# Kernel optimization log

Hardware: AMD Instinct MI355X
Metric: run time of the kernel (lower is better)

Reference implementation:

```python
import jax, jax.numpy as jnp
import numpy as np

B, T, V, H = 32, 512, 1024, 256

def setup_inputs() -> dict:
    key = jax.random.key(0)
    k = jax.random.split(key, 6)
    glorot_x = (6.0 / (V + H)) ** 0.5
    glorot_h = (6.0 / (H + H)) ** 0.5
    glorot_d = (6.0 / (H + V)) ** 0.5
    return {
        "X": jax.random.normal(k[0], (B, T, V), dtype=jnp.float32),
        "Wx": jax.random.uniform(k[1], (V, H), jnp.float32, -glorot_x, glorot_x),
        "Wh": jax.random.uniform(k[2], (H, H), jnp.float32, -glorot_h, glorot_h),
        "b": jnp.zeros((H,), jnp.float32),
        "Wd": jax.random.uniform(k[3], (H, V), jnp.float32, -glorot_d, glorot_d),
        "bd": jnp.zeros((V,), jnp.float32),
    }

def reference(X, Wx, Wh, b, Wd, bd):
    # Precompute input projections for all timesteps: [T, B, H]
    xproj = jnp.einsum('btv,vh->tbh', X, Wx) + b
    h0 = jnp.zeros((X.shape[0], Wh.shape[0]), X.dtype)

    def step(h, xp):
        h_new = jnp.tanh(xp + h @ Wh)  # SimpleRNNCell: tanh(Wx x + Wh h + b)
        return h_new, h_new

    new_state, Ys = jax.lax.scan(step, h0, xproj)  # Ys: [T, B, H]
    Y = jnp.transpose(Ys, (1, 0, 2)).reshape(-1, Wh.shape[0])  # [B*T, H]
    out = jax.nn.softmax(Y @ Wd + bd, axis=-1)  # [B*T, V]
    return out, new_state
```

## Files before the change

### kernel.cpp

```cpp
#include <hip/hip_runtime.h>

typedef float f32x4 __attribute__((ext_vector_type(4)));
typedef float f32x2 __attribute__((ext_vector_type(2)));
typedef _Float16 f16x8 __attribute__((ext_vector_type(8)));
typedef _Float16 f16x4 __attribute__((ext_vector_type(4)));
typedef _Float16 f16x2 __attribute__((ext_vector_type(2)));

__device__ __forceinline__ float tanh_fast(float x) {
  float e = __builtin_amdgcn_exp2f(x * 2.885390081777927f);
  return 1.0f - 2.0f * __builtin_amdgcn_rcpf(e + 1.0f);
}

__global__ __launch_bounds__(256) void k_transpose_cast(
    const float* __restrict__ in, _Float16* __restrict__ outp, int R, int C)
{
  __shared__ float tile[32][33];
  const int tx = threadIdx.x & 31, ty = threadIdx.x >> 5;
  const int tc = blockIdx.x * 32, tr = blockIdx.y * 32;
#pragma unroll
  for (int i = 0; i < 32; i += 8)
    tile[ty + i][tx] = in[(size_t)(tr + ty + i) * C + tc + tx];
  __syncthreads();
#pragma unroll
  for (int i = 0; i < 32; i += 8)
    outp[(size_t)(tc + ty + i) * R + tr + tx] = (_Float16)tile[tx][ty + i];
}

__global__ __launch_bounds__(256) void k_transpose_cast_perm(
    const float* __restrict__ in, _Float16* __restrict__ outp, int R, int C)
{
  __shared__ float tile[32][33];
  const int tx = threadIdx.x & 31, ty = threadIdx.x >> 5;
  const int tc = blockIdx.x * 32, tr = blockIdx.y * 32;
#pragma unroll
  for (int i = 0; i < 32; i += 8)
    tile[ty + i][tx] = in[(size_t)(tr + ty + i) * C + tc + tx];
  __syncthreads();
  const int r = tr + tx;
  const int p = (r & ~31) | ((r & 15) << 1) | ((r >> 4) & 1);
#pragma unroll
  for (int i = 0; i < 32; i += 8)
    outp[(size_t)(tc + ty + i) * R + p] = (_Float16)tile[tx][ty + i];
}

__global__ __launch_bounds__(256) void k_gemm1(
    const float* __restrict__ X, const _Float16* __restrict__ WxT,
    const float* __restrict__ bias, float* __restrict__ xp_packed)
{
  __shared__ _Float16 As[32][72];
  __shared__ _Float16 Bs[256][72];
  const int tid = threadIdx.x;
  const int lane = tid & 63, w = tid >> 6;
  const int l15 = lane & 15, lq = lane >> 4;
  const int m0 = blockIdx.x * 32;
  const int wm = w & 1, wn = w >> 1;

  f32x4 acc[8];
#pragma unroll
  for (int i = 0; i < 8; ++i) acc[i] = (f32x4){0.f, 0.f, 0.f, 0.f};

  for (int kc = 0; kc < 16; ++kc) {
    const int k0 = kc * 64;
#pragma unroll
    for (int it = 0; it < 2; ++it) {
      int q = tid + it * 256;
      int r = q >> 4, k4 = (q & 15) * 4;
      f32x4 v = *(const f32x4*)(X + (size_t)(m0 + r) * 1024 + k0 + k4);
      f16x4 hv;
      hv[0] = (_Float16)v[0]; hv[1] = (_Float16)v[1];
      hv[2] = (_Float16)v[2]; hv[3] = (_Float16)v[3];
      *(f16x4*)(&As[r][k4]) = hv;
    }
#pragma unroll
    for (int it = 0; it < 8; ++it) {
      int q = tid + it * 256;
      int n = q >> 3, k8 = (q & 7) * 8;
      *(f16x8*)(&Bs[n][k8]) = *(const f16x8*)(WxT + (size_t)n * 1024 + k0 + k8);
    }
    __syncthreads();
    f16x8 a[2];
#pragma unroll
    for (int ks = 0; ks < 2; ++ks)
      a[ks] = *(const f16x8*)(&As[wm * 16 + l15][ks * 32 + lq * 8]);
#pragma unroll
    for (int ct = 0; ct < 8; ++ct) {
#pragma unroll
      for (int ks = 0; ks < 2; ++ks) {
        f16x8 bfr = *(const f16x8*)(&Bs[wn * 128 + ct * 16 + l15][ks * 32 + lq * 8]);
        acc[ct] = __builtin_amdgcn_mfma_f32_16x16x32_f16(a[ks], bfr, acc[ct], 0, 0, 0);
      }
    }
    __syncthreads();
  }
#pragma unroll
  for (int ct = 0; ct < 8; ++ct) {
    int ncol = wn * 128 + ct * 16 + l15;
    float bvv = bias[ncol];
    int w_s = ncol >> 5, j_s = (ncol >> 4) & 1, i_s = ncol & 15;
#pragma unroll
    for (int r = 0; r < 4; ++r) {
      int m = m0 + wm * 16 + lq * 4 + r;
      int tt = m & 511, bb = m >> 9;
      int g_s = bb >> 2, lq_s = bb & 3;
      size_t idx = (((size_t)tt * 8 + g_s) * 8 + w_s) * 128 + (lq_s * 16 + i_s) * 2 + j_s;
      xp_packed[idx] = acc[ct][r] + bvv;
    }
  }
}

__global__ __launch_bounds__(512, 2) void k_scan(
    const float* __restrict__ xp_packed,
    const _Float16* __restrict__ WhTp,
    _Float16* __restrict__ Yt,
    float* __restrict__ hT)
{
  __shared__ char hbuf[2][4224];
  const int tid = threadIdx.x;
  const int lane = tid & 63, w = tid >> 6;
  const int l15 = lane & 15, lq = lane >> 4;
  const int g = blockIdx.x;

  for (int i = tid; i < 2112; i += 512) ((float*)hbuf)[i] = 0.f;

  f16x8 bf[2][8];
#pragma unroll
  for (int j = 0; j < 2; ++j)
#pragma unroll
    for (int i = 0; i < 8; ++i) {
      int ks = (w + i) & 7;
      bf[j][i] = *(const f16x8*)(WhTp + (w * 32 + j * 16 + l15) * 256 + ks * 32 + lq * 8);
    }

  char* hz = (char*)&hbuf[0][0];
  const int rd_base = (l15 & 3) * 1056 + w * 64 + lq * 16;
  const int wr_base = lq * 1056 + w * 64 + l15 * 4;
  const bool m1 = (lq & 1) != 0, m2 = (lq & 2) != 0;

  const float* xpb = xp_packed + ((size_t)g * 8 + w) * 128 + lane * 2;
  _Float16* yb = Yt + ((size_t)(g * 4 + lq)) * 256 + w * 32 + l15 * 2;
  float* hTb = hT + (g * 4 + lq) * 256 + w * 32 + l15;

  __syncthreads();

  f32x2 x0 = *(const f32x2*)(xpb);
  f32x2 x1 = *(const f32x2*)(xpb + 8192);

#define SCAN_STEP(T, CUR, X, LAST)                                             \
  {                                                                            \
    const int t = (T);                                                         \
    f16x8 af[8];                                                               \
    af[0] = *(const f16x8*)(hz + rd_base + (CUR) * 4224 + 0 * 64);             \
    asm volatile("" ::: "memory");                                             \
    __builtin_amdgcn_s_barrier();                                              \
    asm volatile("" ::: "memory");                                             \
    _Pragma("unroll")                                                          \
    for (int i = 1; i < 8; ++i)                                                \
      af[i] = *(const f16x8*)(hz + rd_base + (CUR) * 4224 + i * 64);           \
    f32x2 xcur = X;                                                            \
    f32x4 acc[2][4];                                                           \
    _Pragma("unroll")                                                          \
    for (int j = 0; j < 2; ++j) {                                              \
      _Pragma("unroll")                                                        \
      for (int c = 0; c < 4; ++c) {                                            \
        f32x4 zz = {0.f, 0.f, 0.f, 0.f};                                       \
        acc[j][c] = __builtin_amdgcn_mfma_f32_16x16x32_f16(af[2 * c], bf[j][2 * c], zz, 0, 0, 0); \
      }                                                                        \
    }                                                                          \
    {                                                    \
      int tn = t + 2; if (tn > 511) tn = 511;                                  \
      X = *(const f32x2*)(xpb + (size_t)tn * 8192);                            \
    }                                                                          \
    _Pragma("unroll")                                                          \
    for (int j = 0; j < 2; ++j) {                                              \
      _Pragma("unroll")                                                        \
      for (int c = 0; c < 4; ++c)                                              \
        acc[j][c] = __builtin_amdgcn_mfma_f32_16x16x32_f16(af[2 * c + 1], bf[j][2 * c + 1], acc[j][c], 0, 0, 0); \
    }                                                                          \
    f16x2 h2;                                                                  \
    float vv[2];                                                               \
    _Pragma("unroll")                                                          \
    for (int j = 0; j < 2; ++j) {                                              \
      f32x4 s01 = acc[j][0] + acc[j][1];                                       \
      f32x4 s23 = acc[j][2] + acc[j][3];                                       \
      f32x4 s = s01 + s23;                                                     \
      float t0 = m1 ? s[1] : s[0];                                             \
      float t1 = m1 ? s[3] : s[2];                                             \
      float v = tanh_fast((m2 ? t1 : t0) + xcur[j]);                           \
      vv[j] = v;                                                               \
      h2[j] = (_Float16)v;                                                     \
    }                                                                          \
    *(f16x2*)(hz + wr_base + ((CUR) ^ 1) * 4224) = h2;                         \
    *(f16x2*)(hz + wr_base + ((CUR) ^ 1) * 4224 + 512) = h2;                   \
    *(f16x2*)(yb + (size_t)t * 8192) = h2;                                     \
    if (LAST) {                                                                \
      hTb[0] = vv[0];                                                          \
      hTb[16] = vv[1];                                                         \
    }                                                                          \
    asm volatile("s_waitcnt lgkmcnt(0)" ::: "memory");                         \
  }

  SCAN_STEP(0, 0, x0, 0)
  for (int tp = 0; tp < 255; ++tp) {
    SCAN_STEP(2 * tp + 1, 1, x1, 0)
    SCAN_STEP(2 * tp + 2, 0, x0, 0)
  }
  SCAN_STEP(511, 1, x1, 1)
#undef SCAN_STEP
}

__global__ __launch_bounds__(512) void k_gemm3(
    const _Float16* __restrict__ Yt,
    const _Float16* __restrict__ WdTp,
    const float* __restrict__ bd,
    float* __restrict__ out)
{
  __shared__ _Float16 As[16][264];
  __shared__ _Float16 Bs[128][136];
  __shared__ _Float16 lg[16][1040];
  const int tid = threadIdx.x;
  const int lane = tid & 63, w = tid >> 6;
  const int l15 = lane & 15, lq = lane >> 4;
  const int m0 = blockIdx.x * 16;
  const int b = m0 >> 9, t0 = m0 & 511;

  {
    int r = tid >> 5, k8 = (tid & 31) * 8;
    *(f16x8*)(&As[r][k8]) = *(const f16x8*)(Yt + ((size_t)(t0 + r) * 32 + b) * 256 + k8);
  }
  __syncthreads();
  f16x8 a[8];
#pragma unroll
  for (int ks = 0; ks < 8; ++ks)
    a[ks] = *(const f16x8*)(&As[l15][ks * 32 + lq * 8]);

  for (int cc = 0; cc < 8; ++cc) {
    const int c0 = cc * 128;
    const int ncol = c0 + w * 16 + l15;
    f32x4 acc = {0.f, 0.f, 0.f, 0.f};
    __syncthreads();
#pragma unroll
    for (int i = 0; i < 4; ++i) {
      int q = i * 512 + tid;
      int n = q >> 4, k8 = (q & 15) * 8;
      *(f16x8*)(&Bs[n][k8]) = *(const f16x8*)(WdTp + (size_t)(c0 + n) * 256 + k8);
    }
    __syncthreads();
#pragma unroll
    for (int ks = 0; ks < 4; ++ks) {
      f16x8 bfr = *(const f16x8*)(&Bs[w * 16 + l15][ks * 32 + lq * 8]);
      acc = __builtin_amdgcn_mfma_f32_16x16x32_f16(a[ks], bfr, acc, 0, 0, 0);
    }
    __syncthreads();
#pragma unroll
    for (int i = 0; i < 4; ++i) {
      int q = i * 512 + tid;
      int n = q >> 4, k8 = (q & 15) * 8;
      *(f16x8*)(&Bs[n][k8]) = *(const f16x8*)(WdTp + (size_t)(c0 + n) * 256 + 128 + k8);
    }
    __syncthreads();
#pragma unroll
    for (int ks = 4; ks < 8; ++ks) {
      f16x8 bfr = *(const f16x8*)(&Bs[w * 16 + l15][(ks - 4) * 32 + lq * 8]);
      acc = __builtin_amdgcn_mfma_f32_16x16x32_f16(a[ks], bfr, acc, 0, 0, 0);
    }
    float bvv = bd[ncol];
#pragma unroll
    for (int r = 0; r < 4; ++r)
      lg[lq * 4 + r][ncol] = (_Float16)(acc[r] + bvv);
  }
  __syncthreads();

  const int row = tid >> 5, j = tid & 31;
  float mx = -1e30f;
#pragma unroll
  for (int k = 0; k < 32; ++k)
    mx = fmaxf(mx, (float)lg[row][j + k * 32]);
#pragma unroll
  for (int m = 1; m < 32; m <<= 1)
    mx = fmaxf(mx, __shfl_xor(mx, m, 64));
  float s = 0.f;
#pragma unroll
  for (int k = 0; k < 32; ++k)
    s += __builtin_amdgcn_exp2f(((float)lg[row][j + k * 32] - mx) * 1.44269504088896f);
#pragma unroll
  for (int m = 1; m < 32; m <<= 1)
    s += __shfl_xor(s, m, 64);
  const float rinv = __builtin_amdgcn_rcpf(s);
  float* orow = out + (size_t)(m0 + row) * 1024;
#pragma unroll
  for (int k = 0; k < 8; ++k) {
    int c = k * 128 + j * 4;
    f32x4 vv;
#pragma unroll
    for (int u = 0; u < 4; ++u)
      vv[u] = __builtin_amdgcn_exp2f(((float)lg[row][c + u] - mx) * 1.44269504088896f) * rinv;
    *(f32x4*)(orow + c) = vv;
  }
}

extern "C" void kernel_launch(void* const* d_in, const int* in_sizes, int n_in,
                              void* d_out, int out_size, void* d_ws, size_t ws_size,
                              hipStream_t stream) {
  const float* X  = (const float*)d_in[0];
  const float* Wx = (const float*)d_in[1];
  const float* Wh = (const float*)d_in[2];
  const float* bv = (const float*)d_in[3];
  const float* Wd = (const float*)d_in[4];
  const float* bd = (const float*)d_in[5];
  float* out = (float*)d_out;

  char* ws = (char*)d_ws;
  float*    xp_packed = (float*)(ws);
  _Float16* Yt    = (_Float16*)(ws + (16u << 20));
  _Float16* WxT   = (_Float16*)(ws + (24u << 20));
  _Float16* WhTp  = (_Float16*)(ws + (24u << 20) + (512u << 10));
  _Float16* WdTp  = (_Float16*)(ws + (24u << 20) + (640u << 10));

  k_transpose_cast<<<dim3(8, 32), 256, 0, stream>>>(Wx, WxT, 1024, 256);
  k_transpose_cast_perm<<<dim3(8, 8),  256, 0, stream>>>(Wh, WhTp, 256, 256);
  k_transpose_cast_perm<<<dim3(32, 8), 256, 0, stream>>>(Wd, WdTp, 256, 1024);
  k_gemm1<<<dim3(512), 256, 0, stream>>>(X, WxT, bv, xp_packed);
  k_scan<<<dim3(8), 512, 0, stream>>>(xp_packed, WhTp, Yt, out + 16384 * 1024);
  k_gemm3<<<dim3(1024), 512, 0, stream>>>(Yt, WdTp, bd, out);
}
```

Baseline: 321.3 us.

## Fuse input GEMM, scan and output GEMM into one persistent kernel with counters

Merges the three kernels into one persistent launch with 256 blocks split into roles: 8 scan blocks, 184 input-projection blocks and 64 output GEMM+softmax blocks. The roles hand off through global atomic counters per 32-timestep chunk. The scan can start once the first chunks of xproj are ready, and the output GEMM can consume finished chunks while the scan is still running. This hides the GEMM work behind the serial recurrence. It relies on all 256 blocks being co-resident, which risks deadlock if they are not. Spin-waits and the smaller per-block tiles also add overhead.

```diff
diff --git a/kernel.cpp b/kernel.cpp
--- a/kernel.cpp
+++ b/kernel.cpp
@@ -9,6 +9,20 @@
 __device__ __forceinline__ float tanh_fast(float x) {
   float e = __builtin_amdgcn_exp2f(x * 2.885390081777927f);
   return 1.0f - 2.0f * __builtin_amdgcn_rcpf(e + 1.0f);
+}
+
+__device__ __forceinline__ void wait_cnt(int* p, int target) {
+  if (threadIdx.x == 0) {
+    while (__hip_atomic_load(p, __ATOMIC_RELAXED, __HIP_MEMORY_SCOPE_AGENT) < target)
+      __builtin_amdgcn_s_sleep(2);
+    (void)__hip_atomic_load(p, __ATOMIC_ACQUIRE, __HIP_MEMORY_SCOPE_AGENT);
+  }
+  __syncthreads();
+}
+__device__ __forceinline__ void publish_cnt(int* p) {
+  __syncthreads();
+  if (threadIdx.x == 0)
+    (void)__hip_atomic_fetch_add(p, 1, __ATOMIC_RELEASE, __HIP_MEMORY_SCOPE_AGENT);
 }
 
 __global__ __launch_bounds__(256) void k_transpose_cast(
@@ -43,109 +57,48 @@
     outp[(size_t)(tc + ty + i) * R + p] = (_Float16)tile[tx][ty + i];
 }
 
-__global__ __launch_bounds__(256) void k_gemm1(
+__global__ __launch_bounds__(512, 1) void k_fused(
     const float* __restrict__ X, const _Float16* __restrict__ WxT,
-    const float* __restrict__ bias, float* __restrict__ xp_packed)
+    const float* __restrict__ bias, float* __restrict__ xp_packed,
+    const _Float16* __restrict__ WhTp, _Float16* __restrict__ Yt,
+    float* __restrict__ hT,
+    const _Float16* __restrict__ WdTp, const float* __restrict__ bd,
+    float* __restrict__ out, int* cnt1, int* sc)
 {
-  __shared__ _Float16 As[32][72];
-  __shared__ _Float16 Bs[256][72];
+  extern __shared__ char smem[];
+  const int bid = blockIdx.x;
   const int tid = threadIdx.x;
   const int lane = tid & 63, w = tid >> 6;
   const int l15 = lane & 15, lq = lane >> 4;
-  const int m0 = blockIdx.x * 32;
-  const int wm = w & 1, wn = w >> 1;
-
-  f32x4 acc[8];
-#pragma unroll
-  for (int i = 0; i < 8; ++i) acc[i] = (f32x4){0.f, 0.f, 0.f, 0.f};
-
-  for (int kc = 0; kc < 16; ++kc) {
-    const int k0 = kc * 64;
-#pragma unroll
-    for (int it = 0; it < 2; ++it) {
-      int q = tid + it * 256;
-      int r = q >> 4, k4 = (q & 15) * 4;
-      f32x4 v = *(const f32x4*)(X + (size_t)(m0 + r) * 1024 + k0 + k4);
-      f16x4 hv;
-      hv[0] = (_Float16)v[0]; hv[1] = (_Float16)v[1];
-      hv[2] = (_Float16)v[2]; hv[3] = (_Float16)v[3];
-      *(f16x4*)(&As[r][k4]) = hv;
-    }
-#pragma unroll
-    for (int it = 0; it < 8; ++it) {
-      int q = tid + it * 256;
-      int n = q >> 3, k8 = (q & 7) * 8;
-      *(f16x8*)(&Bs[n][k8]) = *(const f16x8*)(WxT + (size_t)n * 1024 + k0 + k8);
-    }
-    __syncthreads();
-    f16x8 a[2];
-#pragma unroll
-    for (int ks = 0; ks < 2; ++ks)
-      a[ks] = *(const f16x8*)(&As[wm * 16 + l15][ks * 32 + lq * 8]);
-#pragma unroll
-    for (int ct = 0; ct < 8; ++ct) {
-#pragma unroll
-      for (int ks = 0; ks < 2; ++ks) {
-        f16x8 bfr = *(const f16x8*)(&Bs[wn * 128 + ct * 16 + l15][ks * 32 + lq * 8]);
-        acc[ct] = __builtin_amdgcn_mfma_f32_16x16x32_f16(a[ks], bfr, acc[ct], 0, 0, 0);
-      }
-    }
-    __syncthreads();
-  }
-#pragma unroll
-  for (int ct = 0; ct < 8; ++ct) {
-    int ncol = wn * 128 + ct * 16 + l15;
-    float bvv = bias[ncol];
-    int w_s = ncol >> 5, j_s = (ncol >> 4) & 1, i_s = ncol & 15;
-#pragma unroll
-    for (int r = 0; r < 4; ++r) {
-      int m = m0 + wm * 16 + lq * 4 + r;
-      int tt = m & 511, bb = m >> 9;
-      int g_s = bb >> 2, lq_s = bb & 3;
-      size_t idx = (((size_t)tt * 8 + g_s) * 8 + w_s) * 128 + (lq_s * 16 + i_s) * 2 + j_s;
-      xp_packed[idx] = acc[ct][r] + bvv;
-    }
-  }
-}
-
-__global__ __launch_bounds__(512, 2) void k_scan(
-    const float* __restrict__ xp_packed,
-    const _Float16* __restrict__ WhTp,
-    _Float16* __restrict__ Yt,
-    float* __restrict__ hT)
-{
-  __shared__ char hbuf[2][4224];
-  const int tid = threadIdx.x;
-  const int lane = tid & 63, w = tid >> 6;
-  const int l15 = lane & 15, lq = lane >> 4;
-  const int g = blockIdx.x;
-
-  for (int i = tid; i < 2112; i += 512) ((float*)hbuf)[i] = 0.f;
-
-  f16x8 bf[2][8];
-#pragma unroll
-  for (int j = 0; j < 2; ++j)
-#pragma unroll
-    for (int i = 0; i < 8; ++i) {
-      int ks = (w + i) & 7;
-      bf[j][i] = *(const f16x8*)(WhTp + (w * 32 + j * 16 + l15) * 256 + ks * 32 + lq * 8);
-    }
-
-  char* hz = (char*)&hbuf[0][0];
-  const int rd_base = (l15 & 3) * 1056 + w * 64 + lq * 16;
-  const int wr_base = lq * 1056 + w * 64 + l15 * 4;
-  const bool m1 = (lq & 1) != 0, m2 = (lq & 2) != 0;
-
-  const float* xpb = xp_packed + ((size_t)g * 8 + w) * 128 + lane * 2;
-  _Float16* yb = Yt + ((size_t)(g * 4 + lq)) * 256 + w * 32 + l15 * 2;
-  float* hTb = hT + (g * 4 + lq) * 256 + w * 32 + l15;
-
-  __syncthreads();
-
-  f32x2 x0 = *(const f32x2*)(xpb);
-  f32x2 x1 = *(const f32x2*)(xpb + 8192);
-
-#define SCAN_STEP(T, CUR, X, LAST)                                             \
+
+  if (bid < 8) {
+    const int g = bid;
+    char* hz = smem;
+    for (int i = tid; i < 2112; i += 512) ((float*)hz)[i] = 0.f;
+
+    f16x8 bf[2][8];
+#pragma unroll
+    for (int j = 0; j < 2; ++j)
+#pragma unroll
+      for (int i = 0; i < 8; ++i) {
+        int ks = (w + i) & 7;
+        bf[j][i] = *(const f16x8*)(WhTp + (w * 32 + j * 16 + l15) * 256 + ks * 32 + lq * 8);
+      }
+
+    const int rd_base = (l15 & 3) * 1056 + w * 64 + lq * 16;
+    const int wr_base = lq * 1056 + w * 64 + l15 * 4;
+    const bool m1 = (lq & 1) != 0, m2 = (lq & 2) != 0;
+
+    const float* xpb = xp_packed + ((size_t)g * 8 + w) * 128 + lane * 2;
+    _Float16* yb = Yt + ((size_t)(g * 4 + lq)) * 256 + w * 32 + l15 * 2;
+    float* hTb = hT + (g * 4 + lq) * 256 + w * 32 + l15;
+
+    wait_cnt(cnt1 + 0, 32);
+
+    f32x2 x0 = *(const f32x2*)(xpb);
+    f32x2 x1 = *(const f32x2*)(xpb + 8192);
+
+#define SCAN_STEP(T, CUR, Xv, LAST)                                            \
   {                                                                            \
     const int t = (T);                                                         \
     f16x8 af[8];                                                               \
@@ -156,25 +109,23 @@
     _Pragma("unroll")                                                          \
     for (int i = 1; i < 8; ++i)                                                \
       af[i] = *(const f16x8*)(hz + rd_base + (CUR) * 4224 + i * 64);           \
-    f32x2 xcur = X;                                                            \
+    f32x2 xcur = Xv;                                                           \
     f32x4 acc[2][4];                                                           \
     _Pragma("unroll")                                                          \
     for (int j = 0; j < 2; ++j) {                                              \
       _Pragma("unroll")                                                        \
-      for (int c = 0; c < 4; ++c) {                                            \
+      for (int c2 = 0; c2 < 4; ++c2) {                                         \
         f32x4 zz = {0.f, 0.f, 0.f, 0.f};                                       \
-        acc[j][c] = __builtin_amdgcn_mfma_f32_16x16x32_f16(af[2 * c], bf[j][2 * c], zz, 0, 0, 0); \
+        acc[j][c2] = __builtin_amdgcn_mfma_f32_16x16x32_f16(af[2 * c2], bf[j][2 * c2], zz, 0, 0, 0); \
       }                                                                        \
     }                                                                          \
-    {                                                    \
-      int tn = t + 2; if (tn > 511) tn = 511;                                  \
-      X = *(const f32x2*)(xpb + (size_t)tn * 8192);                            \
-    }                                                                          \
+    { int tn = t + 2; if (tn > 511) tn = 511;                                  \
+      Xv = *(const f32x2*)(xpb + (size_t)tn * 8192); }                         \
     _Pragma("unroll")                                                          \
     for (int j = 0; j < 2; ++j) {                                              \
       _Pragma("unroll")                                                        \
-      for (int c = 0; c < 4; ++c)                                              \
-        acc[j][c] = __builtin_amdgcn_mfma_f32_16x16x32_f16(af[2 * c + 1], bf[j][2 * c + 1], acc[j][c], 0, 0, 0); \
+      for (int c2 = 0; c2 < 4; ++c2)                                           \
+        acc[j][c2] = __builtin_amdgcn_mfma_f32_16x16x32_f16(af[2 * c2 + 1], bf[j][2 * c2 + 1], acc[j][c2], 0, 0, 0); \
     }                                                                          \
     f16x2 h2;                                                                  \
     float vv[2];                                                               \
@@ -192,109 +143,168 @@
     *(f16x2*)(hz + wr_base + ((CUR) ^ 1) * 4224) = h2;                         \
     *(f16x2*)(hz + wr_base + ((CUR) ^ 1) * 4224 + 512) = h2;                   \
     *(f16x2*)(yb + (size_t)t * 8192) = h2;                                     \
-    if (LAST) {                                                                \
-      hTb[0] = vv[0];                                                          \
-      hTb[16] = vv[1];                                                         \
-    }                                                                          \
+    if (LAST) { hTb[0] = vv[0]; hTb[16] = vv[1]; }                             \
     asm volatile("s_waitcnt lgkmcnt(0)" ::: "memory");                         \
   }
 
-  SCAN_STEP(0, 0, x0, 0)
-  for (int tp = 0; tp < 255; ++tp) {
-    SCAN_STEP(2 * tp + 1, 1, x1, 0)
-    SCAN_STEP(2 * tp + 2, 0, x0, 0)
-  }
-  SCAN_STEP(511, 1, x1, 1)
+    for (int c = 0; c < 16; ++c) {
+      wait_cnt(cnt1 + (c < 15 ? c + 1 : 15), 32);
+      for (int tp = 0; tp < 16; ++tp) {
+        SCAN_STEP(c * 32 + 2 * tp,     0, x0, 0)
+        SCAN_STEP(c * 32 + 2 * tp + 1, 1, x1, (c == 15 && tp == 15))
+      }
+      publish_cnt(sc + c);
+    }
 #undef SCAN_STEP
-}
-
-__global__ __launch_bounds__(512) void k_gemm3(
-    const _Float16* __restrict__ Yt,
-    const _Float16* __restrict__ WdTp,
-    const float* __restrict__ bd,
-    float* __restrict__ out)
-{
-  __shared__ _Float16 As[16][264];
-  __shared__ _Float16 Bs[128][136];
-  __shared__ _Float16 lg[16][1040];
-  const int tid = threadIdx.x;
-  const int lane = tid & 63, w = tid >> 6;
-  const int l15 = lane & 15, lq = lane >> 4;
-  const int m0 = blockIdx.x * 16;
-  const int b = m0 >> 9, t0 = m0 & 511;
-
-  {
-    int r = tid >> 5, k8 = (tid & 31) * 8;
-    *(f16x8*)(&As[r][k8]) = *(const f16x8*)(Yt + ((size_t)(t0 + r) * 32 + b) * 256 + k8);
-  }
-  __syncthreads();
-  f16x8 a[8];
-#pragma unroll
-  for (int ks = 0; ks < 8; ++ks)
-    a[ks] = *(const f16x8*)(&As[l15][ks * 32 + lq * 8]);
-
-  for (int cc = 0; cc < 8; ++cc) {
-    const int c0 = cc * 128;
-    const int ncol = c0 + w * 16 + l15;
-    f32x4 acc = {0.f, 0.f, 0.f, 0.f};
-    __syncthreads();
-#pragma unroll
-    for (int i = 0; i < 4; ++i) {
-      int q = i * 512 + tid;
-      int n = q >> 4, k8 = (q & 15) * 8;
-      *(f16x8*)(&Bs[n][k8]) = *(const f16x8*)(WdTp + (size_t)(c0 + n) * 256 + k8);
+
+  } else if (bid < 192) {
+    const int p = bid - 8;
+    _Float16 (*As)[72] = (_Float16(*)[72])smem;
+    _Float16 (*Bs)[72] = (_Float16(*)[72])(smem + 4608);
+    const int wm = w & 1, wn = w >> 1;
+
+    for (int v = p; v < 512; v += 184) {
+      const int tc = v >> 5, b = v & 31;
+      const int m0 = b * 512 + tc * 32;
+
+      f32x4 acc[4];
+#pragma unroll
+      for (int i = 0; i < 4; ++i) acc[i] = (f32x4){0.f, 0.f, 0.f, 0.f};
+
+      for (int kc = 0; kc < 16; ++kc) {
+        const int k0 = kc * 64;
+        __syncthreads();
+        {
+          int r = tid >> 4, k4 = (tid & 15) * 4;
+          f32x4 vv = *(const f32x4*)(X + (size_t)(m0 + r) * 1024 + k0 + k4);
+          f16x4 hv;
+          hv[0] = (_Float16)vv[0]; hv[1] = (_Float16)vv[1];
+          hv[2] = (_Float16)vv[2]; hv[3] = (_Float16)vv[3];
+          *(f16x4*)(&As[r][k4]) = hv;
+        }
+#pragma unroll
+        for (int it = 0; it < 4; ++it) {
+          int q = tid + it * 512;
+          int n = q >> 3, k8 = (q & 7) * 8;
+          *(f16x8*)(&Bs[n][k8]) = *(const f16x8*)(WxT + (size_t)n * 1024 + k0 + k8);
+        }
+        __syncthreads();
+        f16x8 a[2];
+#pragma unroll
+        for (int ks = 0; ks < 2; ++ks)
+          a[ks] = *(const f16x8*)(&As[wm * 16 + l15][ks * 32 + lq * 8]);
+#pragma unroll
+        for (int ct = 0; ct < 4; ++ct) {
+#pragma unroll
+          for (int ks = 0; ks < 2; ++ks) {
+            f16x8 bfr = *(const f16x8*)(&Bs[wn * 64 + ct * 16 + l15][ks * 32 + lq * 8]);
+            acc[ct] = __builtin_amdgcn_mfma_f32_16x16x32_f16(a[ks], bfr, acc[ct], 0, 0, 0);
+          }
+        }
+      }
+#pragma unroll
+      for (int ct = 0; ct < 4; ++ct) {
+        int ncol = wn * 64 + ct * 16 + l15;
+        float bvv = bias[ncol];
+        int w_s = ncol >> 5, j_s = (ncol >> 4) & 1, i_s = ncol & 15;
+#pragma unroll
+        for (int r = 0; r < 4; ++r) {
+          int m = m0 + wm * 16 + lq * 4 + r;
+          int tt = m & 511, bb = m >> 9;
+          int g_s = bb >> 2, lq_s = bb & 3;
+          size_t idx = (((size_t)tt * 8 + g_s) * 8 + w_s) * 128 + (lq_s * 16 + i_s) * 2 + j_s;
+          xp_packed[idx] = acc[ct][r] + bvv;
+        }
+      }
+      publish_cnt(cnt1 + tc);
     }
-    __syncthreads();
-#pragma unroll
-    for (int ks = 0; ks < 4; ++ks) {
-      f16x8 bfr = *(const f16x8*)(&Bs[w * 16 + l15][ks * 32 + lq * 8]);
-      acc = __builtin_amdgcn_mfma_f32_16x16x32_f16(a[ks], bfr, acc, 0, 0, 0);
+
+  } else {
+    const int q = bid - 192;
+    _Float16 (*As)[264]  = (_Float16(*)[264])smem;
+    _Float16 (*Bs)[136]  = (_Float16(*)[136])(smem + 8448);
+    _Float16 (*lg)[1040] = (_Float16(*)[1040])(smem + 43264);
+
+    for (int v = q; v < 1024; v += 64) {
+      const int b = v & 31, t0 = (v >> 5) * 16;
+      const int m0 = b * 512 + t0;
+      wait_cnt(sc + (t0 >> 5), 8);
+
+      {
+        int r = tid >> 5, k8 = (tid & 31) * 8;
+        *(f16x8*)(&As[r][k8]) = *(const f16x8*)(Yt + ((size_t)(t0 + r) * 32 + b) * 256 + k8);
+      }
+      __syncthreads();
+      f16x8 a[8];
+#pragma unroll
+      for (int ks = 0; ks < 8; ++ks)
+        a[ks] = *(const f16x8*)(&As[l15][ks * 32 + lq * 8]);
+
+      for (int cc = 0; cc < 8; ++cc) {
+        const int c0 = cc * 128;
+        const int ncol = c0 + w * 16 + l15;
+        f32x4 acc = {0.f, 0.f, 0.f, 0.f};
+        __syncthreads();
+#pragma unroll
+        for (int i = 0; i < 4; ++i) {
+          int q2 = i * 512 + tid;
+          int n = q2 >> 4, k8 = (q2 & 15) * 8;
+          *(f16x8*)(&Bs[n][k8]) = *(const f16x8*)(WdTp + (size_t)(c0 + n) * 256 + k8);
+        }
+        __syncthreads();
+#pragma unroll
+        for (int ks = 0; ks < 4; ++ks) {
+          f16x8 bfr = *(const f16x8*)(&Bs[w * 16 + l15][ks * 32 + lq * 8]);
+          acc = __builtin_amdgcn_mfma_f32_16x16x32_f16(a[ks], bfr, acc, 0, 0, 0);
+        }
+        __syncthreads();
+#pragma unroll
+        for (int i = 0; i < 4; ++i) {
+          int q2 = i * 512 + tid;
+          int n = q2 >> 4, k8 = (q2 & 15) * 8;
+          *(f16x8*)(&Bs[n][k8]) = *(const f16x8*)(WdTp + (size_t)(c0 + n) * 256 + 128 + k8);
+        }
+        __syncthreads();
+#pragma unroll
+        for (int ks = 4; ks < 8; ++ks) {
+          f16x8 bfr = *(const f16x8*)(&Bs[w * 16 + l15][(ks - 4) * 32 + lq * 8]);
+          acc = __builtin_amdgcn_mfma_f32_16x16x32_f16(a[ks], bfr, acc, 0, 0, 0);
+        }
+        float bvv = bd[ncol];
+#pragma unroll
+        for (int r = 0; r < 4; ++r)
+          lg[lq * 4 + r][ncol] = (_Float16)(acc[r] + bvv);
+      }
+      __syncthreads();
+
+      const int row = tid >> 5, j = tid & 31;
+      float mx = -1e30f;
+#pragma unroll
+      for (int k = 0; k < 32; ++k)
+        mx = fmaxf(mx, (float)lg[row][j + k * 32]);
+#pragma unroll
+      for (int m = 1; m < 32; m <<= 1)
+        mx = fmaxf(mx, __shfl_xor(mx, m, 64));
+      float s = 0.f;
+#pragma unroll
+      for (int k = 0; k < 32; ++k)
+        s += __builtin_amdgcn_exp2f(((float)lg[row][j + k * 32] - mx) * 1.44269504088896f);
+#pragma unroll
+      for (int m = 1; m < 32; m <<= 1)
+        s += __shfl_xor(s, m, 64);
+      const float rinv = __builtin_amdgcn_rcpf(s);
+      float* orow = out + (size_t)(m0 + row) * 1024;
+#pragma unroll
+      for (int k = 0; k < 8; ++k) {
+        int c = k * 128 + j * 4;
+        f32x4 vv;
+#pragma unroll
+        for (int u = 0; u < 4; ++u)
+          vv[u] = __builtin_amdgcn_exp2f(((float)lg[row][c + u] - mx) * 1.44269504088896f) * rinv;
+        *(f32x4*)(orow + c) = vv;
+      }
+      __syncthreads();
     }
-    __syncthreads();
-#pragma unroll
-    for (int i = 0; i < 4; ++i) {
-      int q = i * 512 + tid;
-      int n = q >> 4, k8 = (q & 15) * 8;
-      *(f16x8*)(&Bs[n][k8]) = *(const f16x8*)(WdTp + (size_t)(c0 + n) * 256 + 128 + k8);
-    }
-    __syncthreads();
-#pragma unroll
-    for (int ks = 4; ks < 8; ++ks) {
-      f16x8 bfr = *(const f16x8*)(&Bs[w * 16 + l15][(ks - 4) * 32 + lq * 8]);
-      acc = __builtin_amdgcn_mfma_f32_16x16x32_f16(a[ks], bfr, acc, 0, 0, 0);
-    }
-    float bvv = bd[ncol];
-#pragma unroll
-    for (int r = 0; r < 4; ++r)
-      lg[lq * 4 + r][ncol] = (_Float16)(acc[r] + bvv);
-  }
-  __syncthreads();
-
-  const int row = tid >> 5, j = tid & 31;
-  float mx = -1e30f;
-#pragma unroll
-  for (int k = 0; k < 32; ++k)
-    mx = fmaxf(mx, (float)lg[row][j + k * 32]);
-#pragma unroll
-  for (int m = 1; m < 32; m <<= 1)
-    mx = fmaxf(mx, __shfl_xor(mx, m, 64));
-  float s = 0.f;
-#pragma unroll
-  for (int k = 0; k < 32; ++k)
-    s += __builtin_amdgcn_exp2f(((float)lg[row][j + k * 32] - mx) * 1.44269504088896f);
-#pragma unroll
-  for (int m = 1; m < 32; m <<= 1)
-    s += __shfl_xor(s, m, 64);
-  const float rinv = __builtin_amdgcn_rcpf(s);
-  float* orow = out + (size_t)(m0 + row) * 1024;
-#pragma unroll
-  for (int k = 0; k < 8; ++k) {
-    int c = k * 128 + j * 4;
-    f32x4 vv;
-#pragma unroll
-    for (int u = 0; u < 4; ++u)
-      vv[u] = __builtin_amdgcn_exp2f(((float)lg[row][c + u] - mx) * 1.44269504088896f) * rinv;
-    *(f32x4*)(orow + c) = vv;
   }
 }
 
@@ -315,11 +325,17 @@
   _Float16* WxT   = (_Float16*)(ws + (24u << 20));
   _Float16* WhTp  = (_Float16*)(ws + (24u << 20) + (512u << 10));
   _Float16* WdTp  = (_Float16*)(ws + (24u << 20) + (640u << 10));
-
+  int*      cnt1  = (int*)(ws + (26u << 20));
+  int*      sc    = cnt1 + 16;
+
+  (void)hipFuncSetAttribute((const void*)k_fused,
+                            hipFuncAttributeMaxDynamicSharedMemorySize, 86016);
+
+  (void)hipMemsetAsync(cnt1, 0, 128, stream);
   k_transpose_cast<<<dim3(8, 32), 256, 0, stream>>>(Wx, WxT, 1024, 256);
   k_transpose_cast_perm<<<dim3(8, 8),  256, 0, stream>>>(Wh, WhTp, 256, 256);
   k_transpose_cast_perm<<<dim3(32, 8), 256, 0, stream>>>(Wd, WdTp, 256, 1024);
-  k_gemm1<<<dim3(512), 256, 0, stream>>>(X, WxT, bv, xp_packed);
-  k_scan<<<dim3(8), 512, 0, stream>>>(xp_packed, WhTp, Yt, out + 16384 * 1024);
-  k_gemm3<<<dim3(1024), 512, 0, stream>>>(Yt, WdTp, bd, out);
-}
+  k_fused<<<dim3(256), dim3(512), 86016, stream>>>(
+      X, WxT, bv, xp_packed, WhTp, Yt, out + 16384 * 1024, WdTp, bd, out,
+      cnt1, sc);
+}
```

Result: slower. 336.0 us (+4.6%).
